# Kernel optimization log

Hardware: AMD Instinct MI355X
Metric: run time of the kernel (lower is better)

The kernel has to match this reference:

```python
import jax, jax.numpy as jnp
import numpy as np

KERNEL = (9, 9, 9)  # box-filter window
KSIZE = KERNEL[0] * KERNEL[1] * KERNEL[2]  # 729
GAMMA = 1.0


def _box_sum(x):
    # x: [B, C, D, H, W] -> channel-sum then 9x9x9 sliding-window sum (SAME pad),
    # exactly matching F.conv3d with an all-ones [1, C, 9,9,9] kernel, pad=4.
    s = jnp.sum(x, axis=1, keepdims=True)  # [B,1,D,H,W]
    return jax.lax.reduce_window(
        s, jnp.asarray(0.0, s.dtype), jax.lax.add,
        window_dimensions=(1, 1) + KERNEL,
        window_strides=(1, 1, 1, 1, 1),
        padding='SAME')


def setup_inputs() -> dict:
    key = jax.random.key(0)
    k1, k2, k3 = jax.random.split(key, 3)
    shape = (2, 1, 160, 160, 160)
    return {
        'input': jax.random.normal(k1, shape, dtype=jnp.float32),
        'target': jax.random.normal(k2, shape, dtype=jnp.float32),
        'flow': jax.random.normal(k3, shape, dtype=jnp.float32),
    }


def reference(input, target, flow):
    # normalize target from (-1, 1) to (0, 1)
    target = (target + 1.0) * 0.5
    w = jax.nn.sigmoid(flow) ** GAMMA  # voxel-wise confidence weight

    T_sum = _box_sum(target)
    I_sum = _box_sum(input)
    TT_sum = _box_sum(target * target)
    II_sum = _box_sum(input * input)
    IT_sum = _box_sum(input * target)

    Ihat = I_sum / KSIZE
    That = T_sum / KSIZE
    cross = IT_sum - Ihat * T_sum - That * I_sum + That * Ihat * KSIZE
    T_var = TT_sum - 2.0 * That * T_sum + That * That * KSIZE
    I_var = II_sum - 2.0 * Ihat * I_sum + Ihat * Ihat * KSIZE

    cc = cross * cross * w / (T_var * I_var + 1e-5)
    return -1.0 * jnp.mean(cc)
```

## Files before the change

### kernel.cpp

```cpp
#include <hip/hip_runtime.h>


constexpr int NB = 2;
constexpr int ND = 160;
constexpr int NH = 160;
constexpr int NW = 160;
constexpr int TH = 16;
constexpr int TW = 16;
constexpr int DCHUNK = 32;
constexpr int NDCH = ND / DCHUNK;
constexpr int NPL = DCHUNK + 8;
constexpr int FS5 = 392;
constexpr float INV_K = 1.0f / 729.0f;
constexpr double INV_COUNT = 1.0 / (double(NB) * ND * NH * NW);

__device__ __forceinline__ void issue_load(
    const float* __restrict__ in, const float* __restrict__ tg,
    int b, int dp, int h0, int w0, int tid,
    float4& iv, float4& tv)
{
    iv = make_float4(0.f, 0.f, 0.f, 0.f);
    tv = make_float4(0.f, 0.f, 0.f, 0.f);
    if (tid < 144 && ((unsigned)dp < (unsigned)ND)) {
        int r = tid / 6;
        int q = tid - r * 6;
        int gh = h0 - 4 + r;
        int gw = w0 - 4 + q * 4;
        if (((unsigned)gh < (unsigned)NH) && ((unsigned)gw < (unsigned)NW)) {
            int base = ((b * ND + dp) * NH + gh) * NW + gw;
            iv = *reinterpret_cast<const float4*>(in + base);
            float4 rv = *reinterpret_cast<const float4*>(tg + base);
            tv.x = fmaf(rv.x, 0.5f, 0.5f);
            tv.y = fmaf(rv.y, 0.5f, 0.5f);
            tv.z = fmaf(rv.z, 0.5f, 0.5f);
            tv.w = fmaf(rv.w, 0.5f, 0.5f);
        }
    }
}

__device__ __forceinline__ void stage(int tid, const float4& iv, const float4& tv,
                                      float* __restrict__ inT, float* __restrict__ tgT)
{
    if (tid < 144) {
        reinterpret_cast<float4*>(inT)[tid] = iv;
        reinterpret_cast<float4*>(tgT)[tid] = tv;
    }
}

__device__ __forceinline__ void step2(int tid, const float* __restrict__ inT,
                                      const float* __restrict__ tgT,
                                      float* __restrict__ tmp5)
{
    int pos = tid;
    #pragma unroll
    for (int rep = 0; rep < 2; ++rep) {
        if (pos < 384) {
            int r = pos >> 4, wo = pos & 15;
            const float* ir = inT + r * 24 + wo;
            const float* tr = tgT + r * 24 + wo;
            float s0 = 0.f, s1 = 0.f, s2 = 0.f, s3 = 0.f, s4 = 0.f;
            #pragma unroll
            for (int k = 0; k < 9; ++k) {
                float ivv = ir[k];
                float t = tr[k];
                s0 += t;
                s1 += ivv;
                s2 = fmaf(t, t, s2);
                s3 = fmaf(ivv, ivv, s3);
                s4 = fmaf(ivv, t, s4);
            }
            int o = r * 16 + wo;
            tmp5[0 * FS5 + o] = s0;
            tmp5[1 * FS5 + o] = s1;
            tmp5[2 * FS5 + o] = s2;
            tmp5[3 * FS5 + o] = s3;
            tmp5[4 * FS5 + o] = s4;
        }
        pos += 256;
    }
}

__device__ __forceinline__ float cc_value(const float S[5], float flv)
{
    float wgt = 1.0f / (1.0f + __expf(-flv));
    float Ts = S[0], Is = S[1], TTs = S[2], IIs = S[3], ITs = S[4];
    float Ihat = Is * INV_K;
    float That = Ts * INV_K;
    float cross = ITs - Ihat * Ts - That * Is + That * Ihat * 729.0f;
    float T_var = TTs - 2.0f * That * Ts + That * That * 729.0f;
    float I_var = IIs - 2.0f * Ihat * Is + Ihat * Ihat * 729.0f;
    return cross * cross * wgt / (T_var * I_var + 1e-5f);
}

__global__ void __launch_bounds__(256)
cc3d_main(const float* __restrict__ in, const float* __restrict__ tg,
          const float* __restrict__ fl, double* __restrict__ acc_out)
{
    __shared__ float inT[24 * 24];
    __shared__ float tgT[24 * 24];
    __shared__ float tmp5[5 * FS5];
    __shared__ float red[4];

    const int tid = threadIdx.x;
    const int w0 = blockIdx.x * TW;
    const int h0 = blockIdx.y * TH;
    const int bz = blockIdx.z;
    const int b  = bz / NDCH;
    const int d0 = (bz - b * NDCH) * DCHUNK;
    const int hh = tid >> 4, ww = tid & 15;

    float ring[45];
    #pragma unroll
    for (int i = 0; i < 45; ++i) ring[i] = 0.f;
    float S[5] = {0.f, 0.f, 0.f, 0.f, 0.f};
    float acc = 0.f;

    float4 iv, tv;
    issue_load(in, tg, b, d0 - 4, h0, w0, tid, iv, tv);

    for (int lb = 0; lb < NPL + 8; lb += 9) {
        #pragma unroll
        for (int li = 0; li < 9; ++li) {
            const int l = lb + li;
            if (l < NPL) {
                const int dp = d0 - 4 + l;
                const bool valid = ((unsigned)dp < (unsigned)ND);
                if (valid) stage(tid, iv, tv, inT, tgT);
                float4 niv, ntv;
                issue_load(in, tg, b, dp + 1, h0, w0, tid, niv, ntv);
                float flv = 0.f;
                if (l >= 8) {
                    int dout = d0 + l - 8;
                    int fidx = ((b * ND + dout) * NH + (h0 + hh)) * NW + (w0 + ww);
                    flv = fl[fidx];
                }
                __syncthreads();
                if (valid) step2(tid, inT, tgT, tmp5);
                __syncthreads();
                #pragma unroll
                for (int f = 0; f < 5; ++f) {
                    float pn = 0.f;
                    if (valid) {
                        const float* bp = tmp5 + f * FS5 + hh * 16 + ww;
                        #pragma unroll
                        for (int k = 0; k < 9; ++k) pn += bp[k * 16];
                    }
                    S[f] += pn - ring[f * 9 + li];
                    ring[f * 9 + li] = pn;
                }
                if (l >= 8) acc += cc_value(S, flv);
                iv = niv; tv = ntv;
            }
        }
    }

    #pragma unroll
    for (int off = 32; off > 0; off >>= 1) acc += __shfl_down(acc, off);
    if ((tid & 63) == 0) red[tid >> 6] = acc;
    __syncthreads();
    if (tid == 0) {
        double v = (double)red[0] + (double)red[1] + (double)red[2] + (double)red[3];
        atomicAdd(acc_out, v);
    }
}

__global__ void cc3d_finalize(const double* __restrict__ acc, float* __restrict__ out)
{
    out[0] = (float)(-(acc[0] * INV_COUNT));
}

extern "C" void kernel_launch(void* const* d_in, const int* in_sizes, int n_in,
                              void* d_out, int out_size, void* d_ws, size_t ws_size,
                              hipStream_t stream)
{
    const float* in = (const float*)d_in[0];
    const float* tg = (const float*)d_in[1];
    const float* fl = (const float*)d_in[2];
    float* out = (float*)d_out;
    double* acc = (double*)d_ws;

    hipMemsetAsync(d_ws, 0, sizeof(double), stream);

    dim3 grid(NW / TW, NH / TH, NB * NDCH);
    cc3d_main<<<grid, dim3(256), 0, stream>>>(in, tg, fl, acc);
    cc3d_finalize<<<1, 1, 0, stream>>>(acc, out);
}
```

Before: 196.2 us.

## Pipeline W/H box passes across planes with sliding-window sums and double buffering

```diff
diff --git a/kernel.cpp b/kernel.cpp
--- a/kernel.cpp
+++ b/kernel.cpp
@@ -10,7 +10,11 @@
 constexpr int DCHUNK = 32;
 constexpr int NDCH = ND / DCHUNK;
 constexpr int NPL = DCHUNK + 8;
-constexpr int FS5 = 392;
+constexpr int NIT = NPL + 2;
+constexpr int TRS = 20;
+constexpr int TFS = 24 * TRS + 8;
+constexpr int PRS = 20;
+constexpr int PFS = 16 * PRS + 8;
 constexpr float INV_K = 1.0f / 729.0f;
 constexpr double INV_COUNT = 1.0 / (double(NB) * ND * NH * NW);
 
@@ -47,36 +51,81 @@
     }
 }
 
-__device__ __forceinline__ void step2(int tid, const float* __restrict__ inT,
-                                      const float* __restrict__ tgT,
-                                      float* __restrict__ tmp5)
-{
-    int pos = tid;
-    #pragma unroll
-    for (int rep = 0; rep < 2; ++rep) {
-        if (pos < 384) {
-            int r = pos >> 4, wo = pos & 15;
-            const float* ir = inT + r * 24 + wo;
-            const float* tr = tgT + r * 24 + wo;
-            float s0 = 0.f, s1 = 0.f, s2 = 0.f, s3 = 0.f, s4 = 0.f;
-            #pragma unroll
-            for (int k = 0; k < 9; ++k) {
-                float ivv = ir[k];
-                float t = tr[k];
-                s0 += t;
-                s1 += ivv;
-                s2 = fmaf(t, t, s2);
-                s3 = fmaf(ivv, ivv, s3);
-                s4 = fmaf(ivv, t, s4);
-            }
-            int o = r * 16 + wo;
-            tmp5[0 * FS5 + o] = s0;
-            tmp5[1 * FS5 + o] = s1;
-            tmp5[2 * FS5 + o] = s2;
-            tmp5[3 * FS5 + o] = s3;
-            tmp5[4 * FS5 + o] = s4;
-        }
-        pos += 256;
+#define W9SLIDE(EXPR, FI)                                                  \
+    {                                                                      \
+        float p0 = (EXPR(0)), p1 = (EXPR(1)), p2 = (EXPR(2)),              \
+              p3 = (EXPR(3)), p4 = (EXPR(4)), p5 = (EXPR(5)),              \
+              p6 = (EXPR(6)), p7 = (EXPR(7)), p8 = (EXPR(8)),              \
+              p9 = (EXPR(9)), p10 = (EXPR(10)), p11 = (EXPR(11));          \
+        float s = p0 + p1 + p2 + p3 + p4 + p5 + p6 + p7 + p8;              \
+        float4 o;                                                          \
+        o.x = s; s += p9 - p0;                                             \
+        o.y = s; s += p10 - p1;                                            \
+        o.z = s; s += p11 - p2;                                            \
+        o.w = s;                                                           \
+        *reinterpret_cast<float4*>(outp + (FI) * TFS) = o;                 \
+    }
+
+__device__ __forceinline__ void step2q(int tid, const float* __restrict__ inT,
+                                       const float* __restrict__ tgT,
+                                       float* __restrict__ t5)
+{
+    if (tid < 96) {
+        const int r = tid >> 2, q = tid & 3;
+        const float4* ip = reinterpret_cast<const float4*>(inT + r * 24 + 4 * q);
+        const float4* tp = reinterpret_cast<const float4*>(tgT + r * 24 + 4 * q);
+        const float4 i0 = ip[0], i1 = ip[1], i2 = ip[2];
+        const float4 t0 = tp[0], t1 = tp[1], t2 = tp[2];
+        const float ia[12] = {i0.x, i0.y, i0.z, i0.w, i1.x, i1.y, i1.z, i1.w,
+                              i2.x, i2.y, i2.z, i2.w};
+        const float ta[12] = {t0.x, t0.y, t0.z, t0.w, t1.x, t1.y, t1.z, t1.w,
+                              t2.x, t2.y, t2.z, t2.w};
+        float* outp = t5 + r * TRS + 4 * q;
+        #define E_T(j)  ta[j]
+        #define E_I(j)  ia[j]
+        #define E_TT(j) (ta[j] * ta[j])
+        #define E_II(j) (ia[j] * ia[j])
+        #define E_IT(j) (ia[j] * ta[j])
+        W9SLIDE(E_T, 0)
+        W9SLIDE(E_I, 1)
+        W9SLIDE(E_TT, 2)
+        W9SLIDE(E_II, 3)
+        W9SLIDE(E_IT, 4)
+        #undef E_T
+        #undef E_I
+        #undef E_TT
+        #undef E_II
+        #undef E_IT
+    }
+}
+
+__device__ __forceinline__ void hpass(int tid, const float* __restrict__ t5,
+                                      float* __restrict__ Pb)
+{
+    if (tid < 80) {
+        const int f = tid >> 4;
+        const int rem = tid & 15;
+        const int wq = rem >> 2, hs = rem & 3;
+        const float* bp = t5 + f * TFS + hs * 4 * TRS + wq * 4;
+        float4 r4[12];
+        #pragma unroll
+        for (int k = 0; k < 12; ++k)
+            r4[k] = *reinterpret_cast<const float4*>(bp + k * TRS);
+        float sx = r4[0].x, sy = r4[0].y, sz = r4[0].z, sw = r4[0].w;
+        #pragma unroll
+        for (int k = 1; k < 9; ++k) {
+            sx += r4[k].x; sy += r4[k].y; sz += r4[k].z; sw += r4[k].w;
+        }
+        float* op = Pb + f * PFS + hs * 4 * PRS + wq * 4;
+        *reinterpret_cast<float4*>(op) = make_float4(sx, sy, sz, sw);
+        #pragma unroll
+        for (int j = 1; j < 4; ++j) {
+            sx += r4[8 + j].x - r4[j - 1].x;
+            sy += r4[8 + j].y - r4[j - 1].y;
+            sz += r4[8 + j].z - r4[j - 1].z;
+            sw += r4[8 + j].w - r4[j - 1].w;
+            *reinterpret_cast<float4*>(op + j * PRS) = make_float4(sx, sy, sz, sw);
+        }
     }
 }
 
@@ -92,13 +141,14 @@
     return cross * cross * wgt / (T_var * I_var + 1e-5f);
 }
 
-__global__ void __launch_bounds__(256)
+__global__ void __launch_bounds__(256, 4)
 cc3d_main(const float* __restrict__ in, const float* __restrict__ tg,
           const float* __restrict__ fl, double* __restrict__ acc_out)
 {
-    __shared__ float inT[24 * 24];
-    __shared__ float tgT[24 * 24];
-    __shared__ float tmp5[5 * FS5];
+    __shared__ __align__(16) float inT[24 * 24];
+    __shared__ __align__(16) float tgT[24 * 24];
+    __shared__ __align__(16) float tmp5[2][5 * TFS];
+    __shared__ __align__(16) float Pb[5 * PFS];
     __shared__ float red[4];
 
     const int tid = threadIdx.x;
@@ -114,42 +164,50 @@
     for (int i = 0; i < 45; ++i) ring[i] = 0.f;
     float S[5] = {0.f, 0.f, 0.f, 0.f, 0.f};
     float acc = 0.f;
-
-    float4 iv, tv;
-    issue_load(in, tg, b, d0 - 4, h0, w0, tid, iv, tv);
-
-    for (int lb = 0; lb < NPL + 8; lb += 9) {
+    float flv = 0.f, flv_next = 0.f;
+
+    float4 civ, ctv;
+    issue_load(in, tg, b, d0 - 4, h0, w0, tid, civ, ctv);
+
+    for (int lb = 0; lb < 45; lb += 9) {
         #pragma unroll
         for (int li = 0; li < 9; ++li) {
             const int l = lb + li;
-            if (l < NPL) {
-                const int dp = d0 - 4 + l;
-                const bool valid = ((unsigned)dp < (unsigned)ND);
-                if (valid) stage(tid, iv, tv, inT, tgT);
-                float4 niv, ntv;
-                issue_load(in, tg, b, dp + 1, h0, w0, tid, niv, ntv);
-                float flv = 0.f;
-                if (l >= 8) {
-                    int dout = d0 + l - 8;
-                    int fidx = ((b * ND + dout) * NH + (h0 + hh)) * NW + (w0 + ww);
-                    flv = fl[fidx];
-                }
+            if (l < NIT) {
+                if (l >= 2) {
+                    const int lm2 = l - 2;
+                    const int dpz = d0 - 4 + lm2;
+                    const bool vz = ((unsigned)dpz < (unsigned)ND);
+                    const int slot = (li + 7) % 9;
+                    #pragma unroll
+                    for (int f = 0; f < 5; ++f) {
+                        float pn = vz ? Pb[f * PFS + hh * PRS + ww] : 0.f;
+                        S[f] += pn - ring[f * 9 + slot];
+                        ring[f * 9 + slot] = pn;
+                    }
+                    if (lm2 >= 8) acc += cc_value(S, flv);
+                }
+                if (l < NPL) stage(tid, civ, ctv, inT, tgT);
                 __syncthreads();
-                if (valid) step2(tid, inT, tgT, tmp5);
+                if (l < NPL) {
+                    const int dpl = d0 - 4 + l;
+                    if ((unsigned)dpl < (unsigned)ND)
+                        step2q(tid, inT, tgT, tmp5[l & 1]);
+                }
+                if (l >= 1 && l <= NPL) {
+                    const int dph = d0 - 4 + (l - 1);
+                    if ((unsigned)dph < (unsigned)ND)
+                        hpass(tid, tmp5[(l - 1) & 1], Pb);
+                }
+                float4 niv = make_float4(0.f, 0.f, 0.f, 0.f), ntv = niv;
+                if (l + 1 < NPL)
+                    issue_load(in, tg, b, d0 - 4 + (l + 1), h0, w0, tid, niv, ntv);
+                if (l >= 9 && l <= 40) {
+                    int dout = d0 + (l - 9);
+                    flv_next = fl[((b * ND + dout) * NH + (h0 + hh)) * NW + (w0 + ww)];
+                }
                 __syncthreads();
-                #pragma unroll
-                for (int f = 0; f < 5; ++f) {
-                    float pn = 0.f;
-                    if (valid) {
-                        const float* bp = tmp5 + f * FS5 + hh * 16 + ww;
-                        #pragma unroll
-                        for (int k = 0; k < 9; ++k) pn += bp[k * 16];
-                    }
-                    S[f] += pn - ring[f * 9 + li];
-                    ring[f * 9 + li] = pn;
-                }
-                if (l >= 8) acc += cc_value(S, flv);
-                iv = niv; tv = ntv;
+                civ = niv; ctv = ntv; flv = flv_next;
             }
         }
     }
```

Result: faster. 176.5 us (-10.0%).
